# Performance work log

Hardware: AMD Instinct MI355X
Metric: run time of the kernel (lower is better)

The kernel has to match this reference:

```python
import jax, jax.numpy as jnp
import numpy as np

K_S = 2  # spatial order
K_T = 3  # temporal localization factor


def setup_inputs() -> dict:
    key = jax.random.key(0)
    ks = jax.random.split(key, 5)
    B, T, N = 8, 12, 250
    return {
        "history_data": jax.random.normal(ks[0], (B, T, N, 128), dtype=jnp.float32),
        "Prior": jax.random.normal(ks[1], (B, T, N, 64), dtype=jnp.float32),
        "Observed": jax.random.normal(ks[2], (B, T, N, 32), dtype=jnp.float32),
        "W_emb": jax.random.normal(ks[3], (224, 64), dtype=jnp.float32) * 0.05,
        "b_emb": jnp.zeros((64,), dtype=jnp.float32),
        "use_X": 1,
    }


def _transition(adj):
    # P = D^{-1} A : faithful to diag-embed @ adj, realized as row scaling
    rowsum = adj.sum(axis=-1) + 1e-9
    d_inv = 1.0 / rowsum
    d_inv = jnp.where(jnp.isinf(d_inv) | jnp.isnan(d_inv), 0.0, d_inv)
    return d_inv[..., :, None] * adj


def _forward(history_data, Prior, Observed, W_emb, b_emb):
    # nodevec: [B,T,N,64]
    nodevec = jnp.tanh(
        jnp.concatenate([history_data, Prior, Observed], axis=-1) @ W_emb + b_emb
    )
    # similarity: [B,T,N,N]
    sim = jax.nn.relu(jnp.einsum("btnd,btmd->btnm", nodevec, nodevec))
    # symmetric normalization D^{-1/2} S D^{-1/2}
    d = (sim.sum(axis=-1) + 1e-9) ** -0.5
    adj = d[..., :, None] * sim * d[..., None, :]
    P1 = jnp.swapaxes(_transition(adj), -2, -1)
    P2 = jnp.swapaxes(_transition(jnp.swapaxes(adj, -2, -1)), -2, -1)
    N = adj.shape[-1]
    mask = 1.0 - jnp.eye(N, dtype=adj.dtype)
    outs = []
    for g in (P1, P2):
        k1 = g
        ordered = [k1 * mask]
        for _k in range(2, K_S + 1):
            k1 = k1 @ g
            ordered.append(k1 * mask)
        for og in ordered:
            B, T, Nn, _ = og.shape
            # st_localization: tile each row K_T times along last dim
            ex = jnp.broadcast_to(og[..., None, :], (B, T, Nn, K_T, Nn))
            outs.append(ex.reshape(B, T, Nn, K_T * Nn))
    return tuple(outs)


def reference(history_data, Prior, Observed, W_emb, b_emb, use_X):
    # use_X == 1 path (fc_x_emb on concatenated features)
    return _forward(history_data, Prior, Observed, W_emb, b_emb)
```

## Files before the change

kernel.cpp:

```cpp
#include <hip/hip_runtime.h>
#include <hip/hip_bf16.h>

#define G_N 96
#define N_N 250
#define N_P 256
#define E_N 64
#define OUT_GSTRIDE (250 * 750)
#define OUT_STRIDE  (96 * 250 * 750)

typedef __attribute__((ext_vector_type(4))) float floatx4;
typedef __attribute__((ext_vector_type(8))) short shortx8;

__device__ __forceinline__ float bf2f(unsigned short u) {
    union { unsigned int i; float f; } v; v.i = ((unsigned int)u) << 16; return v.f;
}
__device__ __forceinline__ unsigned short f2bf(float f) {
    union { float f; unsigned int i; } v; v.f = f;
    unsigned int x = v.i;
    return (unsigned short)((x + 0x7fffu + ((x >> 16) & 1u)) >> 16);
}

__global__ __launch_bounds__(256) void k_embed(
    const float* __restrict__ hist, const float* __restrict__ prior,
    const float* __restrict__ obs, const float* __restrict__ Wemb,
    const float* __restrict__ bemb, unsigned short* __restrict__ nvb)
{
    __shared__ __attribute__((aligned(16))) float Xt[32][68];
    __shared__ __attribute__((aligned(16))) float Wl[32][64];
    const int t  = threadIdx.x;
    const int tx = t & 15, ty = t >> 4;
    const int rr0 = blockIdx.x * 64;
    const int g   = rr0 >> 8;
    const int n0  = rr0 & 255;

    float acc[4][4] = {};

    for (int c = 0; c < 7; ++c) {
        const float* src; int rowlen, off;
        if (c < 4)      { src = hist;  rowlen = 128; off = c << 5; }
        else if (c < 6) { src = prior; rowlen = 64;  off = (c - 4) << 5; }
        else            { src = obs;   rowlen = 32;  off = 0; }
        __syncthreads();
        {
            const int d  = t & 31;
            const int nb = t >> 5;
            #pragma unroll
            for (int p = 0; p < 8; ++p) {
                const int nl = nb + p * 8;
                const int n  = n0 + nl;
                float v = 0.0f;
                if (n < N_N) v = src[(size_t)(g * N_N + n) * rowlen + off + d];
                Xt[d][nl] = v;
            }
        }
        {
            const int e  = t & 63;
            const int db = t >> 6;
            #pragma unroll
            for (int p = 0; p < 8; ++p) {
                const int dl = db + p * 4;
                Wl[dl][e] = Wemb[(c * 32 + dl) * 64 + e];
            }
        }
        __syncthreads();
        #pragma unroll
        for (int k = 0; k < 32; ++k) {
            const float4 av = *(const float4*)&Xt[k][4 * ty];
            const float4 bv = *(const float4*)&Wl[k][4 * tx];
            const float a[4] = {av.x, av.y, av.z, av.w};
            const float b[4] = {bv.x, bv.y, bv.z, bv.w};
            #pragma unroll
            for (int r = 0; r < 4; ++r)
                #pragma unroll
                for (int cc = 0; cc < 4; ++cc)
                    acc[r][cc] = fmaf(a[r], b[cc], acc[r][cc]);
        }
    }
    #pragma unroll
    for (int r = 0; r < 4; ++r) {
        const int nl = 4 * ty + r;
        const int n  = n0 + nl;
        unsigned short* d2 = nvb + ((size_t)g * N_P + (n0 + nl)) * E_N + 4 * tx;
        #pragma unroll
        for (int cc = 0; cc < 4; ++cc) {
            float v = 0.0f;
            if (n < N_N) v = tanhf(acc[r][cc] + bemb[4 * tx + cc]);
            d2[cc] = f2bf(v);
        }
    }
}

__global__ __launch_bounds__(256) void k_sim(
    const unsigned short* __restrict__ nvb, unsigned short* __restrict__ Sb,
    float* __restrict__ rowsum)
{
    const int blk = blockIdx.x;
    const int g   = blk >> 4;
    const int i0  = (blk & 15) << 4;
    const int t    = threadIdx.x;
    const int w    = t >> 6;
    const int lane = t & 63;
    const int m = lane & 15, kg = lane >> 4;

    const shortx8* nvg = (const shortx8*)(nvb + (size_t)g * N_P * E_N);
    const shortx8 a0 = nvg[(i0 + m) * 8 + kg];
    const shortx8 a1 = nvg[(i0 + m) * 8 + 4 + kg];

    floatx4 acc[4];
    const floatx4 zero = {0.f, 0.f, 0.f, 0.f};
    #pragma unroll
    for (int tt = 0; tt < 4; ++tt) {
        const int j = (w << 6) + (tt << 4) + m;
        const shortx8 b0 = nvg[j * 8 + kg];
        const shortx8 b1 = nvg[j * 8 + 4 + kg];
        floatx4 c = zero;
        c = __builtin_amdgcn_mfma_f32_16x16x32_bf16(a0, b0, c, 0, 0, 0);
        c = __builtin_amdgcn_mfma_f32_16x16x32_bf16(a1, b1, c, 0, 0, 0);
        acc[tt] = c;
    }

    float v[4] = {0.f, 0.f, 0.f, 0.f};
    unsigned short* Sg = Sb + (size_t)g * N_P * N_P;
    #pragma unroll
    for (int tt = 0; tt < 4; ++tt) {
        #pragma unroll
        for (int r = 0; r < 4; ++r) {
            float s = acc[tt][r];
            s = s > 0.f ? s : 0.f;
            const int il = (kg << 2) + r;
            const int j  = (w << 6) + (tt << 4) + m;
            Sg[(size_t)(i0 + il) * N_P + j] = f2bf(s);
            v[r] += s;
        }
    }
    #pragma unroll
    for (int r = 0; r < 4; ++r) {
        v[r] += __shfl_xor(v[r], 1);
        v[r] += __shfl_xor(v[r], 2);
        v[r] += __shfl_xor(v[r], 4);
        v[r] += __shfl_xor(v[r], 8);
    }
    __shared__ float rs[4][16];
    if (m == 0) {
        #pragma unroll
        for (int r = 0; r < 4; ++r) rs[w][(kg << 2) + r] = v[r];
    }
    __syncthreads();
    if (t < 16) rowsum[g * N_P + i0 + t] = rs[0][t] + rs[1][t] + rs[2][t] + rs[3][t];
}

__global__ __launch_bounds__(256) void k_trans(
    const unsigned short* __restrict__ Sb, const float* __restrict__ rowsum,
    float* __restrict__ cArr, float* __restrict__ wArr)
{
    const int g  = blockIdx.x >> 2;
    const int i0 = (blockIdx.x & 3) << 6;
    const int t  = threadIdx.x;
    __shared__ float dL[N_P];
    dL[t] = rsqrtf(rowsum[g * N_P + t] + 1e-9f);
    __syncthreads();
    const int i  = i0 + (t >> 2);
    const int j0 = (t & 3) << 6;
    const unsigned short* row = Sb + (size_t)g * N_P * N_P + (size_t)i * N_P + j0;
    float acc = 0.f;
    #pragma unroll
    for (int j = 0; j < 64; ++j) acc = fmaf(bf2f(row[j]), dL[j0 + j], acc);
    acc += __shfl_xor(acc, 1);
    acc += __shfl_xor(acc, 2);
    if ((t & 3) == 0) {
        const float d = dL[i];
        const float r = 1.0f / (d * acc + 1e-9f);
        const float c = r * d;
        cArr[g * N_P + i] = c;
        wArr[g * N_P + i] = c * d;
    }
}

__global__ __launch_bounds__(256) void k_out0(
    const unsigned short* __restrict__ Sb, const float* __restrict__ rowsum,
    const float* __restrict__ cArr, const float* __restrict__ wArr,
    unsigned short* __restrict__ SA, float* __restrict__ out)
{
    const int blk = blockIdx.x;
    const int g   = blk >> 4;
    const int i0  = (blk & 15) << 4;
    const int t   = threadIdx.x;
    __shared__ float cL[N_P], wL[N_P];
    cL[t] = cArr[g * N_P + t];
    wL[t] = wArr[g * N_P + t];
    __syncthreads();
    const unsigned short* Sg = Sb + (size_t)g * N_P * N_P;
    unsigned short* SAg = SA + (size_t)g * N_P * N_P;
    float* o0 = out + (size_t)g * OUT_GSTRIDE;
    float* o2 = out + 2 * (size_t)OUT_STRIDE + (size_t)g * OUT_GSTRIDE;
    #pragma unroll 1
    for (int il = 0; il < 16; ++il) {
        const int i = i0 + il;
        const float dI = rsqrtf(rowsum[g * N_P + i] + 1e-9f);
        const float s  = bf2f(Sg[(size_t)i * N_P + t]);
        SAg[(size_t)i * N_P + t] = f2bf(s * wL[t]);
        if (i < N_N && t < N_N) {
            const float p = (t == i) ? 0.f : dI * s * cL[t];
            const size_t base = (size_t)i * 750 + t;
            o0[base] = p; o0[base + 250] = p; o0[base + 500] = p;
            o2[base] = p; o2[base + 250] = p; o2[base + 500] = p;
        }
    }
}

__global__ __launch_bounds__(256) void k_pp(
    const unsigned short* __restrict__ SA, const unsigned short* __restrict__ Sb,
    const float* __restrict__ rowsum, const float* __restrict__ cArr,
    float* __restrict__ out)
{
    const int blk = blockIdx.x;
    const int g   = blk >> 4;
    const int i0  = ((blk >> 2) & 3) << 6;
    const int j0  = (blk & 3) << 6;
    const int t    = threadIdx.x;
    const int w    = t >> 6;
    const int lane = t & 63;
    const int m = lane & 15, kg = lane >> 4;

    __shared__ __attribute__((aligned(16))) unsigned short As[64][40];
    __shared__ __attribute__((aligned(16))) unsigned short Bs[64][40];
    __shared__ float dRow[64], cCol[64];

    if (t < 64) dRow[t] = rsqrtf(rowsum[g * N_P + i0 + t] + 1e-9f);
    else if (t < 128) cCol[t - 64] = cArr[g * N_P + j0 + (t - 64)];

    const unsigned short* SAg = SA + (size_t)g * N_P * N_P;
    const unsigned short* Sgb = Sb + (size_t)g * N_P * N_P;

    floatx4 acc[4];
    const floatx4 zero = {0.f, 0.f, 0.f, 0.f};
    #pragma unroll
    for (int tt = 0; tt < 4; ++tt) acc[tt] = zero;

    const int sr = t >> 2, sc = t & 3;
    for (int kb = 0; kb < 8; ++kb) {
        __syncthreads();
        *(uint4*)&As[sr][sc * 8] = *(const uint4*)(SAg + (size_t)(i0 + sr) * N_P + kb * 32 + sc * 8);
        *(uint4*)&Bs[sr][sc * 8] = *(const uint4*)(Sgb + (size_t)(j0 + sr) * N_P + kb * 32 + sc * 8);
        __syncthreads();
        const shortx8 a = *(const shortx8*)&As[(w << 4) + m][kg << 3];
        #pragma unroll
        for (int tt = 0; tt < 4; ++tt) {
            const shortx8 b = *(const shortx8*)&Bs[(tt << 4) + m][kg << 3];
            acc[tt] = __builtin_amdgcn_mfma_f32_16x16x32_bf16(a, b, acc[tt], 0, 0, 0);
        }
    }

    float* o1 = out + (size_t)OUT_STRIDE + (size_t)g * OUT_GSTRIDE;
    float* o3 = out + 3 * (size_t)OUT_STRIDE + (size_t)g * OUT_GSTRIDE;
    #pragma unroll
    for (int tt = 0; tt < 4; ++tt) {
        #pragma unroll
        for (int r = 0; r < 4; ++r) {
            const int iL = (w << 4) + (kg << 2) + r;
            const int jL = (tt << 4) + m;
            const int I = i0 + iL, J = j0 + jL;
            if (I < N_N && J < N_N) {
                const float q = (I == J) ? 0.f : acc[tt][r] * dRow[iL] * cCol[jL];
                const size_t base = (size_t)I * 750 + J;
                o1[base] = q; o1[base + 250] = q; o1[base + 500] = q;
                o3[base] = q; o3[base + 250] = q; o3[base + 500] = q;
            }
        }
    }
}

extern "C" void kernel_launch(void* const* d_in, const int* in_sizes, int n_in,
                              void* d_out, int out_size, void* d_ws, size_t ws_size,
                              hipStream_t stream) {
    const float* hist  = (const float*)d_in[0];
    const float* prior = (const float*)d_in[1];
    const float* obs   = (const float*)d_in[2];
    const float* Wemb  = (const float*)d_in[3];
    const float* bemb  = (const float*)d_in[4];
    float* out = (float*)d_out;

    char* p = (char*)d_ws;
    unsigned short* nvb = (unsigned short*)p; p += (size_t)G_N * N_P * E_N * 2;
    unsigned short* Sb  = (unsigned short*)p; p += (size_t)G_N * N_P * N_P * 2;
    unsigned short* SA  = (unsigned short*)p; p += (size_t)G_N * N_P * N_P * 2;
    float* rowsum = (float*)p; p += (size_t)G_N * N_P * 4;
    float* cArr   = (float*)p; p += (size_t)G_N * N_P * 4;
    float* wArr   = (float*)p; p += (size_t)G_N * N_P * 4;

    k_embed<<<dim3(G_N * N_P / 64), dim3(256), 0, stream>>>(hist, prior, obs, Wemb, bemb, nvb);
    k_sim  <<<dim3(G_N * 16),       dim3(256), 0, stream>>>(nvb, Sb, rowsum);
    k_trans<<<dim3(G_N * 4),        dim3(256), 0, stream>>>(Sb, rowsum, cArr, wArr);
    k_out0 <<<dim3(G_N * 16),       dim3(256), 0, stream>>>(Sb, rowsum, cArr, wArr, SA, out);
    k_pp   <<<dim3(G_N * 16),       dim3(256), 0, stream>>>(SA, Sb, rowsum, cArr, out);
}
```

Measured before the change: 441.1 us.

## Fuse column scaling into matmul A-tile, drop SA buffer, use nontemporal stores

```diff
diff --git a/kernel.cpp b/kernel.cpp
--- a/kernel.cpp
+++ b/kernel.cpp
@@ -153,44 +153,47 @@
     const unsigned short* __restrict__ Sb, const float* __restrict__ rowsum,
     float* __restrict__ cArr, float* __restrict__ wArr)
 {
-    const int g  = blockIdx.x >> 2;
-    const int i0 = (blockIdx.x & 3) << 6;
-    const int t  = threadIdx.x;
-    __shared__ float dL[N_P];
+    const int g = blockIdx.x;
+    const int t = threadIdx.x;
+    __shared__ __attribute__((aligned(16))) float dL[N_P];
     dL[t] = rsqrtf(rowsum[g * N_P + t] + 1e-9f);
     __syncthreads();
-    const int i  = i0 + (t >> 2);
-    const int j0 = (t & 3) << 6;
-    const unsigned short* row = Sb + (size_t)g * N_P * N_P + (size_t)i * N_P + j0;
-    float acc = 0.f;
-    #pragma unroll
-    for (int j = 0; j < 64; ++j) acc = fmaf(bf2f(row[j]), dL[j0 + j], acc);
-    acc += __shfl_xor(acc, 1);
-    acc += __shfl_xor(acc, 2);
-    if ((t & 3) == 0) {
-        const float d = dL[i];
-        const float r = 1.0f / (d * acc + 1e-9f);
-        const float c = r * d;
-        cArr[g * N_P + i] = c;
-        wArr[g * N_P + i] = c * d;
-    }
+    const shortx8* row = (const shortx8*)(Sb + (size_t)g * N_P * N_P + (size_t)t * N_P);
+    float a0 = 0.f, a1 = 0.f, a2 = 0.f, a3 = 0.f;
+    #pragma unroll
+    for (int ch = 0; ch < 32; ++ch) {
+        const shortx8 sv = row[ch];
+        const float4 d0 = *(const float4*)&dL[ch * 8];
+        const float4 d1 = *(const float4*)&dL[ch * 8 + 4];
+        a0 = fmaf(bf2f((unsigned short)sv[0]), d0.x, a0);
+        a1 = fmaf(bf2f((unsigned short)sv[1]), d0.y, a1);
+        a2 = fmaf(bf2f((unsigned short)sv[2]), d0.z, a2);
+        a3 = fmaf(bf2f((unsigned short)sv[3]), d0.w, a3);
+        a0 = fmaf(bf2f((unsigned short)sv[4]), d1.x, a0);
+        a1 = fmaf(bf2f((unsigned short)sv[5]), d1.y, a1);
+        a2 = fmaf(bf2f((unsigned short)sv[6]), d1.z, a2);
+        a3 = fmaf(bf2f((unsigned short)sv[7]), d1.w, a3);
+    }
+    const float s  = (a0 + a1) + (a2 + a3);
+    const float d  = dL[t];
+    const float r  = 1.0f / (d * s + 1e-9f);
+    const float c  = r * d;
+    cArr[g * N_P + t] = c;
+    wArr[g * N_P + t] = c * d;
 }
 
 __global__ __launch_bounds__(256) void k_out0(
     const unsigned short* __restrict__ Sb, const float* __restrict__ rowsum,
-    const float* __restrict__ cArr, const float* __restrict__ wArr,
-    unsigned short* __restrict__ SA, float* __restrict__ out)
+    const float* __restrict__ cArr, float* __restrict__ out)
 {
     const int blk = blockIdx.x;
     const int g   = blk >> 4;
     const int i0  = (blk & 15) << 4;
     const int t   = threadIdx.x;
-    __shared__ float cL[N_P], wL[N_P];
+    __shared__ float cL[N_P];
     cL[t] = cArr[g * N_P + t];
-    wL[t] = wArr[g * N_P + t];
     __syncthreads();
     const unsigned short* Sg = Sb + (size_t)g * N_P * N_P;
-    unsigned short* SAg = SA + (size_t)g * N_P * N_P;
     float* o0 = out + (size_t)g * OUT_GSTRIDE;
     float* o2 = out + 2 * (size_t)OUT_STRIDE + (size_t)g * OUT_GSTRIDE;
     #pragma unroll 1
@@ -198,19 +201,22 @@
         const int i = i0 + il;
         const float dI = rsqrtf(rowsum[g * N_P + i] + 1e-9f);
         const float s  = bf2f(Sg[(size_t)i * N_P + t]);
-        SAg[(size_t)i * N_P + t] = f2bf(s * wL[t]);
         if (i < N_N && t < N_N) {
             const float p = (t == i) ? 0.f : dI * s * cL[t];
             const size_t base = (size_t)i * 750 + t;
-            o0[base] = p; o0[base + 250] = p; o0[base + 500] = p;
-            o2[base] = p; o2[base + 250] = p; o2[base + 500] = p;
+            __builtin_nontemporal_store(p, o0 + base);
+            __builtin_nontemporal_store(p, o0 + base + 250);
+            __builtin_nontemporal_store(p, o0 + base + 500);
+            __builtin_nontemporal_store(p, o2 + base);
+            __builtin_nontemporal_store(p, o2 + base + 250);
+            __builtin_nontemporal_store(p, o2 + base + 500);
         }
     }
 }
 
 __global__ __launch_bounds__(256) void k_pp(
-    const unsigned short* __restrict__ SA, const unsigned short* __restrict__ Sb,
-    const float* __restrict__ rowsum, const float* __restrict__ cArr,
+    const unsigned short* __restrict__ Sb, const float* __restrict__ rowsum,
+    const float* __restrict__ cArr, const float* __restrict__ wArr,
     float* __restrict__ out)
 {
     const int blk = blockIdx.x;
@@ -225,12 +231,13 @@
     __shared__ __attribute__((aligned(16))) unsigned short As[64][40];
     __shared__ __attribute__((aligned(16))) unsigned short Bs[64][40];
     __shared__ float dRow[64], cCol[64];
+    __shared__ __attribute__((aligned(16))) float wL[N_P];
 
     if (t < 64) dRow[t] = rsqrtf(rowsum[g * N_P + i0 + t] + 1e-9f);
     else if (t < 128) cCol[t - 64] = cArr[g * N_P + j0 + (t - 64)];
-
-    const unsigned short* SAg = SA + (size_t)g * N_P * N_P;
-    const unsigned short* Sgb = Sb + (size_t)g * N_P * N_P;
+    wL[t] = wArr[g * N_P + t];
+
+    const unsigned short* Sg = Sb + (size_t)g * N_P * N_P;
 
     floatx4 acc[4];
     const floatx4 zero = {0.f, 0.f, 0.f, 0.f};
@@ -240,14 +247,21 @@
     const int sr = t >> 2, sc = t & 3;
     for (int kb = 0; kb < 8; ++kb) {
         __syncthreads();
-        *(uint4*)&As[sr][sc * 8] = *(const uint4*)(SAg + (size_t)(i0 + sr) * N_P + kb * 32 + sc * 8);
-        *(uint4*)&Bs[sr][sc * 8] = *(const uint4*)(Sgb + (size_t)(j0 + sr) * N_P + kb * 32 + sc * 8);
+        *(uint4*)&As[sr][sc * 8] = *(const uint4*)(Sg + (size_t)(i0 + sr) * N_P + kb * 32 + sc * 8);
+        *(uint4*)&Bs[sr][sc * 8] = *(const uint4*)(Sg + (size_t)(j0 + sr) * N_P + kb * 32 + sc * 8);
         __syncthreads();
         const shortx8 a = *(const shortx8*)&As[(w << 4) + m][kg << 3];
+        const float4 w0 = *(const float4*)&wL[kb * 32 + (kg << 3)];
+        const float4 w1 = *(const float4*)&wL[kb * 32 + (kg << 3) + 4];
+        const float wv[8] = {w0.x, w0.y, w0.z, w0.w, w1.x, w1.y, w1.z, w1.w};
+        shortx8 aw;
+        #pragma unroll
+        for (int u = 0; u < 8; ++u)
+            aw[u] = (short)f2bf(bf2f((unsigned short)a[u]) * wv[u]);
         #pragma unroll
         for (int tt = 0; tt < 4; ++tt) {
             const shortx8 b = *(const shortx8*)&Bs[(tt << 4) + m][kg << 3];
-            acc[tt] = __builtin_amdgcn_mfma_f32_16x16x32_bf16(a, b, acc[tt], 0, 0, 0);
+            acc[tt] = __builtin_amdgcn_mfma_f32_16x16x32_bf16(aw, b, acc[tt], 0, 0, 0);
         }
     }
 
@@ -263,8 +277,12 @@
             if (I < N_N && J < N_N) {
                 const float q = (I == J) ? 0.f : acc[tt][r] * dRow[iL] * cCol[jL];
                 const size_t base = (size_t)I * 750 + J;
-                o1[base] = q; o1[base + 250] = q; o1[base + 500] = q;
-                o3[base] = q; o3[base + 250] = q; o3[base + 500] = q;
+                __builtin_nontemporal_store(q, o1 + base);
+                __builtin_nontemporal_store(q, o1 + base + 250);
+                __builtin_nontemporal_store(q, o1 + base + 500);
+                __builtin_nontemporal_store(q, o3 + base);
+                __builtin_nontemporal_store(q, o3 + base + 250);
+                __builtin_nontemporal_store(q, o3 + base + 500);
             }
         }
     }
@@ -283,14 +301,13 @@
     char* p = (char*)d_ws;
     unsigned short* nvb = (unsigned short*)p; p += (size_t)G_N * N_P * E_N * 2;
     unsigned short* Sb  = (unsigned short*)p; p += (size_t)G_N * N_P * N_P * 2;
-    unsigned short* SA  = (unsigned short*)p; p += (size_t)G_N * N_P * N_P * 2;
     float* rowsum = (float*)p; p += (size_t)G_N * N_P * 4;
     float* cArr   = (float*)p; p += (size_t)G_N * N_P * 4;
     float* wArr   = (float*)p; p += (size_t)G_N * N_P * 4;
 
     k_embed<<<dim3(G_N * N_P / 64), dim3(256), 0, stream>>>(hist, prior, obs, Wemb, bemb, nvb);
     k_sim  <<<dim3(G_N * 16),       dim3(256), 0, stream>>>(nvb, Sb, rowsum);
-    k_trans<<<dim3(G_N * 4),        dim3(256), 0, stream>>>(Sb, rowsum, cArr, wArr);
-    k_out0 <<<dim3(G_N * 16),       dim3(256), 0, stream>>>(Sb, rowsum, cArr, wArr, SA, out);
-    k_pp   <<<dim3(G_N * 16),       dim3(256), 0, stream>>>(SA, Sb, rowsum, cArr, out);
-}
+    k_trans<<<dim3(G_N),            dim3(256), 0, stream>>>(Sb, rowsum, cArr, wArr);
+    k_out0 <<<dim3(G_N * 16),       dim3(256), 0, stream>>>(Sb, rowsum, cArr, out);
+    k_pp   <<<dim3(G_N * 16),       dim3(256), 0, stream>>>(Sb, rowsum, cArr, wArr, out);
+}
```

Result: slower. 499.9 us (+13.3%).
